# Optimization experiments

Hardware: AMD Instinct MI355X
Metric: run time of the kernel (lower is better)

The kernel has to match this reference:

```python
import jax, jax.numpy as jnp
import numpy as np

L, B, D, H = 1024, 128, 256, 256


def setup_inputs() -> dict:
    key = jax.random.key(0)
    k1, k2, k3, k4, k5 = jax.random.split(key, 5)
    bound_x = 1.0 / np.sqrt(D)
    bound_h = 1.0 / np.sqrt(H)
    return {
        "x": jax.random.normal(k1, (L, B, D), dtype=jnp.float32),
        "h": jnp.zeros((B, H), dtype=jnp.float32),
        "Wx_w": jax.random.uniform(k2, (H, D), jnp.float32, -bound_x, bound_x),
        "Wx_b": jax.random.uniform(k3, (H,), jnp.float32, -bound_x, bound_x),
        "Wh_w": jax.random.uniform(k4, (H, H), jnp.float32, -bound_h, bound_h),
        "Wh_b": jax.random.uniform(k5, (H,), jnp.float32, -bound_h, bound_h),
    }


def reference(x, h, Wx_w, Wx_b, Wh_w, Wh_b):
    # Precompute input projections for all timesteps in one big GEMM:
    # [L,B,D] @ [D,H] -> [L,B,H]
    xproj = jnp.einsum('lbd,hd->lbh', x, Wx_w) + Wx_b

    def step(h_prev, xp_t):
        # Elman step: h_t = tanh(Wx x_t + b_x + Wh h_{t-1} + b_h)
        h_new = jnp.tanh(xp_t + h_prev @ Wh_w.T + Wh_b)
        return h_new, h_new

    h_final, hAll = jax.lax.scan(step, h, xproj)
    return hAll, h_final
```

## Files before the change

kernel.cpp:

```cpp
#include <hip/hip_runtime.h>
#include <cstddef>

#define L_SEQ 1024
#define B_SZ  128
#define D_SZ  256
#define H_SZ  256

#define KT  16
#define LDA 132

__global__ __launch_bounds__(256) void xproj_gemm(
    const float* __restrict__ x, const float* __restrict__ Wx,
    const float* __restrict__ bx, float* __restrict__ out)
{
    __shared__ float sA[KT][LDA];
    __shared__ float sB[KT][LDA];

    const int tm  = blockIdx.x;
    const int tn  = blockIdx.y;
    const int tid = threadIdx.x;
    const int tx  = tid & 15;
    const int ty  = tid >> 4;
    const int srow = tid >> 2;
    const int skq  = tid & 3;

    const float* __restrict__ Ag = x  + (size_t)(tm * 128 + srow) * D_SZ + skq * 4;
    const float* __restrict__ Bg = Wx + (size_t)(tn * 128 + srow) * D_SZ + skq * 4;

    float c[2][2][4][4];
    #pragma unroll
    for (int mc = 0; mc < 2; ++mc)
        #pragma unroll
        for (int nc = 0; nc < 2; ++nc)
            #pragma unroll
            for (int i = 0; i < 4; ++i)
                #pragma unroll
                for (int j = 0; j < 4; ++j) c[mc][nc][i][j] = 0.0f;

    for (int kt = 0; kt < D_SZ / KT; ++kt) {
        float4 av0 = *reinterpret_cast<const float4*>(Ag + kt * KT);
        float4 av1 = *reinterpret_cast<const float4*>(Ag + (size_t)64 * D_SZ + kt * KT);
        float4 bv0 = *reinterpret_cast<const float4*>(Bg + kt * KT);
        float4 bv1 = *reinterpret_cast<const float4*>(Bg + (size_t)64 * D_SZ + kt * KT);
        __syncthreads();
        sA[skq * 4 + 0][srow] = av0.x; sA[skq * 4 + 1][srow] = av0.y;
        sA[skq * 4 + 2][srow] = av0.z; sA[skq * 4 + 3][srow] = av0.w;
        sA[skq * 4 + 0][64 + srow] = av1.x; sA[skq * 4 + 1][64 + srow] = av1.y;
        sA[skq * 4 + 2][64 + srow] = av1.z; sA[skq * 4 + 3][64 + srow] = av1.w;
        sB[skq * 4 + 0][srow] = bv0.x; sB[skq * 4 + 1][srow] = bv0.y;
        sB[skq * 4 + 2][srow] = bv0.z; sB[skq * 4 + 3][srow] = bv0.w;
        sB[skq * 4 + 0][64 + srow] = bv1.x; sB[skq * 4 + 1][64 + srow] = bv1.y;
        sB[skq * 4 + 2][64 + srow] = bv1.z; sB[skq * 4 + 3][64 + srow] = bv1.w;
        __syncthreads();
        #pragma unroll
        for (int kk = 0; kk < KT; ++kk) {
            float4 am0 = *reinterpret_cast<const float4*>(&sA[kk][ty * 4]);
            float4 am1 = *reinterpret_cast<const float4*>(&sA[kk][64 + ty * 4]);
            float4 bn0 = *reinterpret_cast<const float4*>(&sB[kk][tx * 4]);
            float4 bn1 = *reinterpret_cast<const float4*>(&sB[kk][64 + tx * 4]);
            float aa[2][4] = {{am0.x, am0.y, am0.z, am0.w}, {am1.x, am1.y, am1.z, am1.w}};
            float bb[2][4] = {{bn0.x, bn0.y, bn0.z, bn0.w}, {bn1.x, bn1.y, bn1.z, bn1.w}};
            #pragma unroll
            for (int mc = 0; mc < 2; ++mc)
                #pragma unroll
                for (int nc = 0; nc < 2; ++nc)
                    #pragma unroll
                    for (int i = 0; i < 4; ++i)
                        #pragma unroll
                        for (int j = 0; j < 4; ++j)
                            c[mc][nc][i][j] = fmaf(aa[mc][i], bb[nc][j], c[mc][nc][i][j]);
        }
    }

    #pragma unroll
    for (int nc = 0; nc < 2; ++nc) {
        float4 bias = *reinterpret_cast<const float4*>(bx + tn * 128 + nc * 64 + tx * 4);
        #pragma unroll
        for (int mc = 0; mc < 2; ++mc)
            #pragma unroll
            for (int i = 0; i < 4; ++i) {
                float4 v;
                v.x = c[mc][nc][i][0] + bias.x;
                v.y = c[mc][nc][i][1] + bias.y;
                v.z = c[mc][nc][i][2] + bias.z;
                v.w = c[mc][nc][i][3] + bias.w;
                *reinterpret_cast<float4*>(
                    out + (size_t)(tm * 128 + mc * 64 + ty * 4 + i) * H_SZ
                        + tn * 128 + nc * 64 + tx * 4) = v;
            }
    }
}

#define SLICE_W 40

typedef float f2 __attribute__((ext_vector_type(2)));

#define PKFMA(acc, w, h) \
    asm("v_pk_fma_f32 %0, %1, %2, %0" : "+v"(acc) : "v"(w), "v"(h))

template <int CTRL>
__device__ __forceinline__ float dpp_add(float v) {
    int y = __builtin_amdgcn_mov_dpp(__float_as_int(v), CTRL, 0xf, 0xf, true);
    return v + __int_as_float(y);
}
__device__ __forceinline__ float swz_xor4_add(float v) {
    int y = __builtin_amdgcn_ds_swizzle(__float_as_int(v), 0x101F);
    return v + __int_as_float(y);
}
__device__ __forceinline__ float red8(f2 a) {
    float v = a.x + a.y;
    v = dpp_add<0xB1>(v);
    v = dpp_add<0x4E>(v);
    v = swz_xor4_add(v);
    return v;
}
__device__ __forceinline__ float fast_tanh(float x) {
    float e = __expf(2.0f * x);
    return 1.0f - 2.0f * __builtin_amdgcn_rcpf(e + 1.0f);
}

#define DECLQ(c, q) \
    f2 w##c##_##q##l = r##c[2 * (q)], w##c##_##q##h = r##c[2 * (q) + 1];
#define DECLC(c) \
    DECLQ(c,0) DECLQ(c,1) DECLQ(c,2) DECLQ(c,3) \
    DECLQ(c,4) DECLQ(c,5) DECLQ(c,6) DECLQ(c,7)

#define FMAQ(q) { \
    float4 hv = hv4[q]; \
    f2 hlo = {hv.x, hv.y}; \
    f2 hhi = {hv.z, hv.w}; \
    PKFMA(a0, w0_##q##l, hlo); PKFMA(a0, w0_##q##h, hhi); \
    PKFMA(a1, w1_##q##l, hlo); PKFMA(a1, w1_##q##h, hhi); \
    PKFMA(a2, w2_##q##l, hlo); PKFMA(a2, w2_##q##h, hhi); \
    PKFMA(a3, w3_##q##l, hlo); PKFMA(a3, w3_##q##h, hhi); }

__global__ __launch_bounds__(512)
__attribute__((amdgpu_waves_per_eu(2, 2)))
void rnn_scan(
    const float* __restrict__ h0, const float* __restrict__ Wh,
    const float* __restrict__ bh, float* __restrict__ out)
{
    __shared__ __align__(16) float hs[2][8 * SLICE_W];

    const int b    = blockIdx.x;
    const int tid  = threadIdx.x;
    const int lane = tid & 63;
    const int wave = tid >> 6;
    const int ks   = lane & 7;
    const int jg   = wave * 8 + (lane >> 3);

    const f2* r0 = reinterpret_cast<const f2*>(Wh + (size_t)(jg +   0) * H_SZ + ks * 32);
    const f2* r1 = reinterpret_cast<const f2*>(Wh + (size_t)(jg +  64) * H_SZ + ks * 32);
    const f2* r2 = reinterpret_cast<const f2*>(Wh + (size_t)(jg + 128) * H_SZ + ks * 32);
    const f2* r3 = reinterpret_cast<const f2*>(Wh + (size_t)(jg + 192) * H_SZ + ks * 32);
    DECLC(0) DECLC(1) DECLC(2) DECLC(3)

    const float bj0 = bh[jg +   0];
    const float bj1 = bh[jg +  64];
    const float bj2 = bh[jg + 128];
    const float bj3 = bh[jg + 192];

    if (tid < H_SZ) {
        hs[0][(tid >> 5) * SLICE_W + (tid & 31)] = h0[(size_t)b * H_SZ + tid];
    }
    __syncthreads();

    float* __restrict__ outb = out + (size_t)b * H_SZ;
    const size_t tstr = (size_t)B_SZ * H_SZ;

    float xp0 = outb[jg +   0];
    float xp1 = outb[jg +  64];
    float xp2 = outb[jg + 128];
    float xp3 = outb[jg + 192];

    float hn0 = 0.f, hn1 = 0.f, hn2 = 0.f, hn3 = 0.f;
    int cur = 0;
    for (int t = 0; t < L_SEQ; ++t) {
        const size_t nb = (size_t)(t + 1) * tstr;
        float nxp0 = outb[nb + jg +   0];
        float nxp1 = outb[nb + jg +  64];
        float nxp2 = outb[nb + jg + 128];
        float nxp3 = outb[nb + jg + 192];

        f2 a0 = {0.f, 0.f}, a1 = {0.f, 0.f}, a2 = {0.f, 0.f}, a3 = {0.f, 0.f};
        const float4* hv4 = reinterpret_cast<const float4*>(&hs[cur][ks * SLICE_W]);
        FMAQ(0) FMAQ(1) FMAQ(2) FMAQ(3) FMAQ(4) FMAQ(5) FMAQ(6) FMAQ(7)

        float s0 = red8(a0);
        float s1 = red8(a1);
        float s2 = red8(a2);
        float s3 = red8(a3);

        hn0 = fast_tanh(xp0 + bj0 + s0);
        hn1 = fast_tanh(xp1 + bj1 + s1);
        hn2 = fast_tanh(xp2 + bj2 + s2);
        hn3 = fast_tanh(xp3 + bj3 + s3);

        if (ks == 0) {
            const size_t tb = (size_t)t * tstr;
            outb[tb + jg +   0] = hn0;
            outb[tb + jg +  64] = hn1;
            outb[tb + jg + 128] = hn2;
            outb[tb + jg + 192] = hn3;
            float* hw = hs[cur ^ 1];
            const int base = (jg >> 5) * SLICE_W + (jg & 31);
            hw[base + 0 * (2 * SLICE_W)] = hn0;
            hw[base + 1 * (2 * SLICE_W)] = hn1;
            hw[base + 2 * (2 * SLICE_W)] = hn2;
            hw[base + 3 * (2 * SLICE_W)] = hn3;
        }
        __syncthreads();
        cur ^= 1;
        xp0 = nxp0; xp1 = nxp1; xp2 = nxp2; xp3 = nxp3;
    }

    if (ks == 0) {
        float* hf = out + (size_t)L_SEQ * tstr + (size_t)b * H_SZ;
        hf[jg +   0] = hn0;
        hf[jg +  64] = hn1;
        hf[jg + 128] = hn2;
        hf[jg + 192] = hn3;
    }
}

extern "C" void kernel_launch(void* const* d_in, const int* in_sizes, int n_in,
                              void* d_out, int out_size, void* d_ws, size_t ws_size,
                              hipStream_t stream) {
    const float* x    = (const float*)d_in[0];
    const float* h0   = (const float*)d_in[1];
    const float* Wx_w = (const float*)d_in[2];
    const float* Wx_b = (const float*)d_in[3];
    const float* Wh_w = (const float*)d_in[4];
    const float* Wh_b = (const float*)d_in[5];
    float* out = (float*)d_out;

    (void)in_sizes; (void)n_in; (void)d_ws; (void)ws_size; (void)out_size;

    dim3 grid1((L_SEQ * B_SZ) / 128, H_SZ / 128);
    xproj_gemm<<<grid1, 256, 0, stream>>>(x, Wx_w, Wx_b, out);

    rnn_scan<<<dim3(B_SZ), 512, 0, stream>>>(h0, Wh_w, Wh_b, out);
}
```

Measured before the change: 1.115 ms.

## Deepen xproj prefetch, use DPP row reduction, lighter barrier, nontemporal stores

The recurrent kernel now prefetches input projections two timesteps ahead instead of one, so global load latency is hidden behind more work. The final reduction step uses a DPP row operation in place of ds_swizzle, and __syncthreads is replaced with an explicit lgkmcnt wait plus s_barrier that does not wait on outstanding global loads. Stores of hidden states become nontemporal. The custom barrier relies on the prefetch loads not being needed before the barrier; the DPP control 0x141 must match the intended xor-4 lane pattern, otherwise the reduction is wrong.

```diff
diff --git a/kernel.cpp b/kernel.cpp
--- a/kernel.cpp
+++ b/kernel.cpp
@@ -103,20 +103,22 @@
     int y = __builtin_amdgcn_mov_dpp(__float_as_int(v), CTRL, 0xf, 0xf, true);
     return v + __int_as_float(y);
 }
-__device__ __forceinline__ float swz_xor4_add(float v) {
-    int y = __builtin_amdgcn_ds_swizzle(__float_as_int(v), 0x101F);
-    return v + __int_as_float(y);
-}
 __device__ __forceinline__ float red8(f2 a) {
     float v = a.x + a.y;
     v = dpp_add<0xB1>(v);
     v = dpp_add<0x4E>(v);
-    v = swz_xor4_add(v);
+    v = dpp_add<0x141>(v);
     return v;
 }
 __device__ __forceinline__ float fast_tanh(float x) {
     float e = __expf(2.0f * x);
     return 1.0f - 2.0f * __builtin_amdgcn_rcpf(e + 1.0f);
+}
+
+__device__ __forceinline__ void lds_barrier() {
+    asm volatile("s_waitcnt lgkmcnt(0)" ::: "memory");
+    __builtin_amdgcn_s_barrier();
+    asm volatile("" ::: "memory");
 }
 
 #define DECLQ(c, q) \
@@ -172,15 +174,19 @@
     float xp1 = outb[jg +  64];
     float xp2 = outb[jg + 128];
     float xp3 = outb[jg + 192];
+    float xq0 = outb[tstr + jg +   0];
+    float xq1 = outb[tstr + jg +  64];
+    float xq2 = outb[tstr + jg + 128];
+    float xq3 = outb[tstr + jg + 192];
+    const float* pre = outb + 2 * tstr;
 
     float hn0 = 0.f, hn1 = 0.f, hn2 = 0.f, hn3 = 0.f;
     int cur = 0;
     for (int t = 0; t < L_SEQ; ++t) {
-        const size_t nb = (size_t)(t + 1) * tstr;
-        float nxp0 = outb[nb + jg +   0];
-        float nxp1 = outb[nb + jg +  64];
-        float nxp2 = outb[nb + jg + 128];
-        float nxp3 = outb[nb + jg + 192];
+        float n0 = pre[jg +   0];
+        float n1 = pre[jg +  64];
+        float n2 = pre[jg + 128];
+        float n3 = pre[jg + 192];
 
         f2 a0 = {0.f, 0.f}, a1 = {0.f, 0.f}, a2 = {0.f, 0.f}, a3 = {0.f, 0.f};
         const float4* hv4 = reinterpret_cast<const float4*>(&hs[cur][ks * SLICE_W]);
@@ -198,10 +204,10 @@
 
         if (ks == 0) {
             const size_t tb = (size_t)t * tstr;
-            outb[tb + jg +   0] = hn0;
-            outb[tb + jg +  64] = hn1;
-            outb[tb + jg + 128] = hn2;
-            outb[tb + jg + 192] = hn3;
+            __builtin_nontemporal_store(hn0, &outb[tb + jg +   0]);
+            __builtin_nontemporal_store(hn1, &outb[tb + jg +  64]);
+            __builtin_nontemporal_store(hn2, &outb[tb + jg + 128]);
+            __builtin_nontemporal_store(hn3, &outb[tb + jg + 192]);
             float* hw = hs[cur ^ 1];
             const int base = (jg >> 5) * SLICE_W + (jg & 31);
             hw[base + 0 * (2 * SLICE_W)] = hn0;
@@ -209,9 +215,11 @@
             hw[base + 2 * (2 * SLICE_W)] = hn2;
             hw[base + 3 * (2 * SLICE_W)] = hn3;
         }
-        __syncthreads();
+        lds_barrier();
         cur ^= 1;
-        xp0 = nxp0; xp1 = nxp1; xp2 = nxp2; xp3 = nxp3;
+        xp0 = xq0; xp1 = xq1; xp2 = xq2; xp3 = xq3;
+        xq0 = n0;  xq1 = n1;  xq2 = n2;  xq3 = n3;
+        if (t + 3 < L_SEQ) pre += tstr;
     }
 
     if (ks == 0) {
```

Measured after the change: 1.100 ms. About the same (-1.3%).
